# Kernel optimization log

Hardware: AMD Instinct MI355X
Metric: run time of the kernel (lower is better)

Reference implementation:

```python
import jax, jax.numpy as jnp
import numpy as np

F = 256      # n_features
N = 128      # n_nodes
B = 4096     # batch


def setup_inputs() -> dict:
    key = jax.random.key(0)
    ks = jax.random.split(key, 11)
    s = lambda *sh: 1.0 / np.sqrt(sh[-2]) if len(sh) >= 2 else 1.0
    x = jax.random.normal(ks[0], (B, F), dtype=jnp.float32)
    # Block-diagonal weights: [F, in, out] per stage; biases [F, out]
    w1 = jax.random.normal(ks[1], (F, 1, N), dtype=jnp.float32)
    b1 = jax.random.normal(ks[2], (F, N), dtype=jnp.float32) * 0.01
    w2 = jax.random.normal(ks[3], (F, N, N), dtype=jnp.float32) / np.sqrt(N)
    b2 = jax.random.normal(ks[4], (F, N), dtype=jnp.float32) * 0.01
    w3 = jax.random.normal(ks[5], (F, N, N), dtype=jnp.float32) / np.sqrt(N)
    b3 = jax.random.normal(ks[6], (F, N), dtype=jnp.float32) * 0.01
    w4 = jax.random.normal(ks[7], (F, N, 1), dtype=jnp.float32) / np.sqrt(N)
    b4 = jax.random.normal(ks[8], (F, 1), dtype=jnp.float32) * 0.01
    # Final linear: [F, 1] weight, [1] bias
    lr_w = jax.random.normal(ks[9], (F, 1), dtype=jnp.float32) / np.sqrt(F)
    lr_b = jax.random.normal(ks[10], (1,), dtype=jnp.float32) * 0.01
    return {"x": x, "w1": w1, "b1": b1, "w2": w2, "b2": b2,
            "w3": w3, "b3": b3, "w4": w4, "b4": b4,
            "lr_w": lr_w, "lr_b": lr_b}


def reference(x, w1, b1, w2, b2, w3, b3, w4, b4, lr_w, lr_b):
    # Per-feature block-diagonal MLP chain with ReLU between stages.
    # x: [B, F] -> view each feature as a 1-dim input to its own subnet.
    h = x[:, :, None]                                   # [B, F, 1]
    h = jax.nn.relu(jnp.einsum('bfi,fio->bfo', h, w1) + b1)   # [B, F, N]
    h = jax.nn.relu(jnp.einsum('bfi,fio->bfo', h, w2) + b2)   # [B, F, N]
    h = jax.nn.relu(jnp.einsum('bfi,fio->bfo', h, w3) + b3)   # [B, F, N]
    h = jnp.einsum('bfi,fio->bfo', h, w4) + b4                # [B, F, 1]
    x_pre = h[:, :, 0]                                        # [B, F]
    return x_pre @ lr_w + lr_b                                # [B, 1]
```

## Files before the change

kernel.cpp:

```cpp
#include <hip/hip_runtime.h>
#include <hip/hip_bf16.h>

#define F_DIM 256
#define N_DIM 128
#define B_DIM 4096

typedef float f32x4v __attribute__((ext_vector_type(4)));
typedef float f32x16v __attribute__((ext_vector_type(16)));
typedef short s16x8 __attribute__((ext_vector_type(8)));
typedef unsigned int u32x4v __attribute__((ext_vector_type(4)));

#define PIN(x) asm("" : "+v"(x))

__device__ __forceinline__ unsigned short f2bf(float f) {
  union { float f; unsigned u; } v; v.f = f;
  unsigned r = v.u + 0x7fffu + ((v.u >> 16) & 1u);
  return (unsigned short)(r >> 16);
}

__device__ __forceinline__ unsigned pk2(float a, float b) {
  union { __hip_bfloat16 h[2]; unsigned u; } v;
  v.h[0] = __float2bfloat16(a);
  v.h[1] = __float2bfloat16(b);
  return v.u;
}

__device__ __forceinline__ void gload16(const void* g, void* l) {
  __builtin_amdgcn_global_load_lds(
      (const __attribute__((address_space(1))) unsigned int*)g,
      (__attribute__((address_space(3))) unsigned int*)l, 16, 0, 0);
}

__device__ __forceinline__ s16x8 frag1(unsigned d) {
  u32x4v v = {d, 0u, 0u, 0u};
  return __builtin_bit_cast(s16x8, v);
}

struct frag2 { s16x8 lo, hi; };

__device__ __forceinline__ frag2 cvt2(f32x16v a) {
  unsigned P[8];
#pragma unroll
  for (int q = 0; q < 8; ++q)
    P[q] = pk2(fmaxf(a[2 * q], 0.f), fmaxf(a[2 * q + 1], 0.f));
  u32x4v lo = {P[0], P[1], P[2], P[3]};
  u32x4v hh = {P[4], P[5], P[6], P[7]};
  frag2 r;
  r.lo = __builtin_bit_cast(s16x8, lo);
  r.hi = __builtin_bit_cast(s16x8, hh);
  return r;
}

__global__ void prep_w(const float* __restrict__ w2, const float* __restrict__ w3,
                       unsigned int* __restrict__ wTs) {
  __shared__ float tile[128 * 130];
  int m = blockIdx.x;
  const float* src = (m < 256) ? (w2 + (size_t)m * 16384)
                               : (w3 + (size_t)(m - 256) * 16384);
  int t = threadIdx.x;
  for (int k = 0; k < 64; ++k) {
    int idx = k * 256 + t;
    int i = idx >> 7, o = idx & 127;
    tile[o * 130 + i] = src[idx];
  }
  __syncthreads();
  unsigned int* dst = wTs + (size_t)m * 8192;
  for (int k = 0; k < 32; ++k) {
    int idx = k * 256 + t;
    int o = idx >> 6, i2 = idx & 63;
    unsigned pk = (unsigned)f2bf(tile[o * 130 + 2 * i2]) |
                  ((unsigned)f2bf(tile[o * 130 + 2 * i2 + 1]) << 16);
    int w = i2 & 7;
    int i2p = (i2 & ~7) + ((w >> 1) & 1) * 4 + (w & 1) + (((w >> 2) & 1) << 1);
    dst[(o * 64) + (i2p ^ ((o & 15) << 2))] = pk;
  }
}

__global__ void prep_x(const float* __restrict__ x, float* __restrict__ xT) {
  __shared__ float tile[64][65];
  int btile = blockIdx.x & 63;
  int ftile = blockIdx.x >> 6;
  int t = threadIdx.x;
  for (int k = 0; k < 16; ++k) {
    int idx = k * 256 + t;
    int r = idx >> 6, c = idx & 63;
    tile[r][c] = x[(size_t)(btile * 64 + r) * F_DIM + ftile * 64 + c];
  }
  __syncthreads();
  for (int k = 0; k < 16; ++k) {
    int idx = k * 256 + t;
    int fr = idx >> 6, br = idx & 63;
    xT[(size_t)(ftile * 64 + fr) * B_DIM + btile * 64 + br] = tile[br][fr];
  }
}

__global__ __launch_bounds__(256, 2) void mlp_chain(
    const float* __restrict__ xT, const float* __restrict__ w1,
    const float* __restrict__ b1, const float* __restrict__ b2,
    const float* __restrict__ b3, const float* __restrict__ w4,
    const float* __restrict__ b4, const unsigned int* __restrict__ wTs,
    float* __restrict__ xp) {
  __shared__ __align__(16) char Wb[2][128 * 256];
  __shared__ __align__(16) float w4l[N_DIM];

  const int f  = blockIdx.x >> 2;
  const int qt = blockIdx.x & 3;
  const int t  = threadIdx.x;
  const int lane = t & 63, wid = t >> 6;
  const int c32 = lane & 31, hi = lane >> 5;

  {
    const char* s2 = (const char*)(wTs + (size_t)f * 8192);
    const char* s3 = (const char*)(wTs + (size_t)(256 + f) * 8192);
#pragma unroll
    for (int c = 0; c < 8; ++c) {
      int off = (wid * 8 + c) * 1024;
      gload16(s2 + off + lane * 16, &Wb[0][off]);
    }
#pragma unroll
    for (int c = 0; c < 8; ++c) {
      int off = (wid * 8 + c) * 1024;
      gload16(s3 + off + lane * 16, &Wb[1][off]);
    }
    if (t < 32) *(f32x4v*)&w4l[t * 4] = *(const f32x4v*)&w4[f * N_DIM + t * 4];
  }

  unsigned a1d[4], a2d[4], a3d[4];
#pragma unroll
  for (int it = 0; it < 4; ++it) {
    int i = it * 32 + c32;
    float w1v = w1[f * N_DIM + i], b1v = b1[f * N_DIM + i];
    float b2v = b2[f * N_DIM + i], b3v = b3[f * N_DIM + i];
    a1d[it] = hi ? 0u : pk2(w1v, b1v);
    a2d[it] = hi ? 0u : pk2(0.f, b2v);
    a3d[it] = hi ? 0u : pk2(0.f, b3v);
  }
  const float b4f = b4[f];
  const float* xcol = xT + (size_t)f * B_DIM + qt * 1024;
  float* xprow = xp + (size_t)f * B_DIM + qt * 1024;

  const int wbase = c32 * 256 + (((lane & 15) ^ hi) << 4);

  __syncthreads();

  const f32x16v zero = {0.f, 0.f, 0.f, 0.f, 0.f, 0.f, 0.f, 0.f,
                        0.f, 0.f, 0.f, 0.f, 0.f, 0.f, 0.f, 0.f};

  float xvA = xcol[wid * 64 + c32];
  float xvB = xcol[wid * 64 + 32 + c32];
#pragma unroll 1
  for (int itb = 0; itb < 4; ++itb) {
    const int bb = itb * 256 + wid * 64;
    s16x8 BxA = frag1(hi ? 0u : pk2(xvA, 1.0f));
    s16x8 BxB = frag1(hi ? 0u : pk2(xvB, 1.0f));
    float xvA_n = (itb < 3) ? xcol[bb + 256 + c32] : 0.f;
    float xvB_n = (itb < 3) ? xcol[bb + 256 + 32 + c32] : 0.f;

    s16x8 h1A[8], h1B[8];
#pragma unroll
    for (int it = 0; it < 4; ++it) {
      f32x16v hA = __builtin_amdgcn_mfma_f32_32x32x16_bf16(frag1(a1d[it]), BxA,
                                                           zero, 0, 0, 0);
      frag2 rA = cvt2(hA);
      h1A[2 * it] = rA.lo;  h1A[2 * it + 1] = rA.hi;
      PIN(h1A[2 * it]);  PIN(h1A[2 * it + 1]);
      f32x16v hB = __builtin_amdgcn_mfma_f32_32x32x16_bf16(frag1(a1d[it]), BxB,
                                                           zero, 0, 0, 0);
      frag2 rB = cvt2(hB);
      h1B[2 * it] = rB.lo;  h1B[2 * it + 1] = rB.hi;
      PIN(h1B[2 * it]);  PIN(h1B[2 * it + 1]);
    }

    s16x8 h2A[8], h2B[8];
#pragma unroll
    for (int nt = 0; nt < 4; ++nt) {
      f32x16v a2A = __builtin_amdgcn_mfma_f32_32x32x16_bf16(frag1(a2d[nt]), BxA,
                                                            zero, 0, 0, 0);
      f32x16v a2B = __builtin_amdgcn_mfma_f32_32x32x16_bf16(frag1(a2d[nt]), BxB,
                                                            zero, 0, 0, 0);
#pragma unroll
      for (int m = 0; m < 8; ++m) {
        s16x8 af = *(const s16x8*)(&Wb[0][0] + nt * 8192 + (wbase ^ (m << 5)));
        a2A = __builtin_amdgcn_mfma_f32_32x32x16_bf16(af, h1A[m], a2A, 0, 0, 0);
        a2B = __builtin_amdgcn_mfma_f32_32x32x16_bf16(af, h1B[m], a2B, 0, 0, 0);
      }
      frag2 rA = cvt2(a2A);
      h2A[2 * nt] = rA.lo;  h2A[2 * nt + 1] = rA.hi;
      PIN(h2A[2 * nt]);  PIN(h2A[2 * nt + 1]);
      frag2 rB = cvt2(a2B);
      h2B[2 * nt] = rB.lo;  h2B[2 * nt + 1] = rB.hi;
      PIN(h2B[2 * nt]);  PIN(h2B[2 * nt + 1]);
    }

    float pA = 0.f, pB = 0.f;
#pragma unroll
    for (int n3 = 0; n3 < 4; ++n3) {
      f32x16v a3A = __builtin_amdgcn_mfma_f32_32x32x16_bf16(frag1(a3d[n3]), BxA,
                                                            zero, 0, 0, 0);
      f32x16v a3B = __builtin_amdgcn_mfma_f32_32x32x16_bf16(frag1(a3d[n3]), BxB,
                                                            zero, 0, 0, 0);
#pragma unroll
      for (int k = 0; k < 8; ++k) {
        s16x8 af = *(const s16x8*)(&Wb[1][0] + n3 * 8192 + (wbase ^ (k << 5)));
        a3A = __builtin_amdgcn_mfma_f32_32x32x16_bf16(af, h2A[k], a3A, 0, 0, 0);
        a3B = __builtin_amdgcn_mfma_f32_32x32x16_bf16(af, h2B[k], a3B, 0, 0, 0);
      }
#pragma unroll
      for (int q = 0; q < 4; ++q) {
        f32x4v wv = *(const f32x4v*)&w4l[n3 * 32 + q * 8 + hi * 4];
#pragma unroll
        for (int i = 0; i < 4; ++i) {
          pA = fmaf(fmaxf(a3A[4 * q + i], 0.f), wv[i], pA);
          pB = fmaf(fmaxf(a3B[4 * q + i], 0.f), wv[i], pB);
        }
      }
    }
    pA += __shfl_xor(pA, 32, 64);
    pB += __shfl_xor(pB, 32, 64);
    if (hi == 0) {
      xprow[bb + c32]      = pA + b4f;
      xprow[bb + 32 + c32] = pB + b4f;
    }
    xvA = xvA_n;
    xvB = xvB_n;
  }
}

__global__ void final_reduce(const float* __restrict__ xp,
                             const float* __restrict__ lr_w,
                             const float* __restrict__ lr_b,
                             float* __restrict__ out) {
  __shared__ float lw[F_DIM];
  __shared__ float part[4][64];
  int t = threadIdx.x;
  if (t < F_DIM) lw[t] = lr_w[t];
  __syncthreads();
  int q = t >> 6, bl = t & 63;
  int b = blockIdx.x * 64 + bl;
  float acc = 0.f;
#pragma unroll 8
  for (int j = 0; j < 64; ++j) {
    int ff = q * 64 + j;
    acc += xp[(size_t)ff * B_DIM + b] * lw[ff];
  }
  part[q][bl] = acc;
  __syncthreads();
  if (q == 0)
    out[b] = part[0][bl] + part[1][bl] + part[2][bl] + part[3][bl] + lr_b[0];
}

extern "C" void kernel_launch(void* const* d_in, const int* in_sizes, int n_in,
                              void* d_out, int out_size, void* d_ws, size_t ws_size,
                              hipStream_t stream) {
  (void)in_sizes; (void)n_in; (void)out_size; (void)ws_size;
  const float* x    = (const float*)d_in[0];
  const float* w1   = (const float*)d_in[1];
  const float* b1   = (const float*)d_in[2];
  const float* w2   = (const float*)d_in[3];
  const float* b2   = (const float*)d_in[4];
  const float* w3   = (const float*)d_in[5];
  const float* b3   = (const float*)d_in[6];
  const float* w4   = (const float*)d_in[7];
  const float* b4   = (const float*)d_in[8];
  const float* lr_w = (const float*)d_in[9];
  const float* lr_b = (const float*)d_in[10];
  float* out = (float*)d_out;

  char* ws = (char*)d_ws;
  unsigned int* wTs = (unsigned int*)ws;
  float* xT = (float*)(ws + (16u << 20));
  float* xp = (float*)(ws + (16u << 20) + (4u << 20));

  prep_w<<<512, 256, 0, stream>>>(w2, w3, wTs);
  prep_x<<<256, 256, 0, stream>>>(x, xT);
  mlp_chain<<<1024, 256, 0, stream>>>(xT, w1, b1, b2, b3, w4, b4, wTs, xp);
  final_reduce<<<64, 256, 0, stream>>>(xp, lr_w, lr_b, out);
}
```

Baseline: 102.1 us.

## Interleave two output tiles per MFMA chain, raise MFMA priority, pack ReLU

Layers 2 and 3 now process two output column tiles at once, giving four independent MFMA accumulator chains. This hides MFMA dependency latency and shares each h fragment across more MFMAs. s_setprio brackets the MFMA loops so waves issuing matrix work get priority, and the LDS offsets are precomputed and pinned in registers. ReLU is applied after bf16 packing via v_pk_max_i16, which is valid because negative bf16 values compare below zero as signed 16-bit integers. The cost is higher register pressure from the extra live accumulators.

```diff
diff --git a/kernel.cpp b/kernel.cpp
--- a/kernel.cpp
+++ b/kernel.cpp
@@ -41,8 +41,10 @@
 __device__ __forceinline__ frag2 cvt2(f32x16v a) {
   unsigned P[8];
 #pragma unroll
-  for (int q = 0; q < 8; ++q)
-    P[q] = pk2(fmaxf(a[2 * q], 0.f), fmaxf(a[2 * q + 1], 0.f));
+  for (int q = 0; q < 8; ++q) {
+    unsigned pk = pk2(a[2 * q], a[2 * q + 1]);
+    asm("v_pk_max_i16 %0, %1, 0" : "=v"(P[q]) : "v"(pk));
+  }
   u32x4v lo = {P[0], P[1], P[2], P[3]};
   u32x4v hh = {P[4], P[5], P[6], P[7]};
   frag2 r;
@@ -140,6 +142,10 @@
   float* xprow = xp + (size_t)f * B_DIM + qt * 1024;
 
   const int wbase = c32 * 256 + (((lane & 15) ^ hi) << 4);
+  int va[8];
+#pragma unroll
+  for (int m = 0; m < 8; ++m) { va[m] = wbase ^ (m << 5); PIN(va[m]); }
+  const char* wb = &Wb[0][0];
 
   __syncthreads();
 
@@ -173,45 +179,74 @@
 
     s16x8 h2A[8], h2B[8];
 #pragma unroll
-    for (int nt = 0; nt < 4; ++nt) {
-      f32x16v a2A = __builtin_amdgcn_mfma_f32_32x32x16_bf16(frag1(a2d[nt]), BxA,
-                                                            zero, 0, 0, 0);
-      f32x16v a2B = __builtin_amdgcn_mfma_f32_32x32x16_bf16(frag1(a2d[nt]), BxB,
-                                                            zero, 0, 0, 0);
+    for (int ntp = 0; ntp < 2; ++ntp) {
+      const int nt0 = 2 * ntp, nt1 = nt0 + 1;
+      f32x16v u0A = __builtin_amdgcn_mfma_f32_32x32x16_bf16(frag1(a2d[nt0]), BxA,
+                                                            zero, 0, 0, 0);
+      f32x16v u0B = __builtin_amdgcn_mfma_f32_32x32x16_bf16(frag1(a2d[nt0]), BxB,
+                                                            zero, 0, 0, 0);
+      f32x16v u1A = __builtin_amdgcn_mfma_f32_32x32x16_bf16(frag1(a2d[nt1]), BxA,
+                                                            zero, 0, 0, 0);
+      f32x16v u1B = __builtin_amdgcn_mfma_f32_32x32x16_bf16(frag1(a2d[nt1]), BxB,
+                                                            zero, 0, 0, 0);
+      __builtin_amdgcn_s_setprio(1);
 #pragma unroll
       for (int m = 0; m < 8; ++m) {
-        s16x8 af = *(const s16x8*)(&Wb[0][0] + nt * 8192 + (wbase ^ (m << 5)));
-        a2A = __builtin_amdgcn_mfma_f32_32x32x16_bf16(af, h1A[m], a2A, 0, 0, 0);
-        a2B = __builtin_amdgcn_mfma_f32_32x32x16_bf16(af, h1B[m], a2B, 0, 0, 0);
+        s16x8 af0 = *(const s16x8*)(wb + va[m] + nt0 * 8192);
+        s16x8 af1 = *(const s16x8*)(wb + va[m] + nt1 * 8192);
+        u0A = __builtin_amdgcn_mfma_f32_32x32x16_bf16(af0, h1A[m], u0A, 0, 0, 0);
+        u0B = __builtin_amdgcn_mfma_f32_32x32x16_bf16(af0, h1B[m], u0B, 0, 0, 0);
+        u1A = __builtin_amdgcn_mfma_f32_32x32x16_bf16(af1, h1A[m], u1A, 0, 0, 0);
+        u1B = __builtin_amdgcn_mfma_f32_32x32x16_bf16(af1, h1B[m], u1B, 0, 0, 0);
       }
-      frag2 rA = cvt2(a2A);
-      h2A[2 * nt] = rA.lo;  h2A[2 * nt + 1] = rA.hi;
-      PIN(h2A[2 * nt]);  PIN(h2A[2 * nt + 1]);
-      frag2 rB = cvt2(a2B);
-      h2B[2 * nt] = rB.lo;  h2B[2 * nt + 1] = rB.hi;
-      PIN(h2B[2 * nt]);  PIN(h2B[2 * nt + 1]);
+      __builtin_amdgcn_s_setprio(0);
+      frag2 r0A = cvt2(u0A);
+      h2A[2 * nt0] = r0A.lo;  h2A[2 * nt0 + 1] = r0A.hi;
+      PIN(h2A[2 * nt0]);  PIN(h2A[2 * nt0 + 1]);
+      frag2 r0B = cvt2(u0B);
+      h2B[2 * nt0] = r0B.lo;  h2B[2 * nt0 + 1] = r0B.hi;
+      PIN(h2B[2 * nt0]);  PIN(h2B[2 * nt0 + 1]);
+      frag2 r1A = cvt2(u1A);
+      h2A[2 * nt1] = r1A.lo;  h2A[2 * nt1 + 1] = r1A.hi;
+      PIN(h2A[2 * nt1]);  PIN(h2A[2 * nt1 + 1]);
+      frag2 r1B = cvt2(u1B);
+      h2B[2 * nt1] = r1B.lo;  h2B[2 * nt1 + 1] = r1B.hi;
+      PIN(h2B[2 * nt1]);  PIN(h2B[2 * nt1 + 1]);
     }
 
     float pA = 0.f, pB = 0.f;
 #pragma unroll
-    for (int n3 = 0; n3 < 4; ++n3) {
-      f32x16v a3A = __builtin_amdgcn_mfma_f32_32x32x16_bf16(frag1(a3d[n3]), BxA,
-                                                            zero, 0, 0, 0);
-      f32x16v a3B = __builtin_amdgcn_mfma_f32_32x32x16_bf16(frag1(a3d[n3]), BxB,
-                                                            zero, 0, 0, 0);
+    for (int n3p = 0; n3p < 2; ++n3p) {
+      const int n30 = 2 * n3p, n31 = n30 + 1;
+      f32x16v v0A = __builtin_amdgcn_mfma_f32_32x32x16_bf16(frag1(a3d[n30]), BxA,
+                                                            zero, 0, 0, 0);
+      f32x16v v0B = __builtin_amdgcn_mfma_f32_32x32x16_bf16(frag1(a3d[n30]), BxB,
+                                                            zero, 0, 0, 0);
+      f32x16v v1A = __builtin_amdgcn_mfma_f32_32x32x16_bf16(frag1(a3d[n31]), BxA,
+                                                            zero, 0, 0, 0);
+      f32x16v v1B = __builtin_amdgcn_mfma_f32_32x32x16_bf16(frag1(a3d[n31]), BxB,
+                                                            zero, 0, 0, 0);
+      __builtin_amdgcn_s_setprio(1);
 #pragma unroll
       for (int k = 0; k < 8; ++k) {
-        s16x8 af = *(const s16x8*)(&Wb[1][0] + n3 * 8192 + (wbase ^ (k << 5)));
-        a3A = __builtin_amdgcn_mfma_f32_32x32x16_bf16(af, h2A[k], a3A, 0, 0, 0);
-        a3B = __builtin_amdgcn_mfma_f32_32x32x16_bf16(af, h2B[k], a3B, 0, 0, 0);
+        s16x8 af0 = *(const s16x8*)(wb + va[k] + 32768 + n30 * 8192);
+        s16x8 af1 = *(const s16x8*)(wb + va[k] + 32768 + n31 * 8192);
+        v0A = __builtin_amdgcn_mfma_f32_32x32x16_bf16(af0, h2A[k], v0A, 0, 0, 0);
+        v0B = __builtin_amdgcn_mfma_f32_32x32x16_bf16(af0, h2B[k], v0B, 0, 0, 0);
+        v1A = __builtin_amdgcn_mfma_f32_32x32x16_bf16(af1, h2A[k], v1A, 0, 0, 0);
+        v1B = __builtin_amdgcn_mfma_f32_32x32x16_bf16(af1, h2B[k], v1B, 0, 0, 0);
       }
+      __builtin_amdgcn_s_setprio(0);
 #pragma unroll
       for (int q = 0; q < 4; ++q) {
-        f32x4v wv = *(const f32x4v*)&w4l[n3 * 32 + q * 8 + hi * 4];
+        f32x4v wv0 = *(const f32x4v*)&w4l[n30 * 32 + q * 8 + hi * 4];
+        f32x4v wv1 = *(const f32x4v*)&w4l[n31 * 32 + q * 8 + hi * 4];
 #pragma unroll
         for (int i = 0; i < 4; ++i) {
-          pA = fmaf(fmaxf(a3A[4 * q + i], 0.f), wv[i], pA);
-          pB = fmaf(fmaxf(a3B[4 * q + i], 0.f), wv[i], pB);
+          pA = fmaf(fmaxf(v0A[4 * q + i], 0.f), wv0[i], pA);
+          pB = fmaf(fmaxf(v0B[4 * q + i], 0.f), wv0[i], pB);
+          pA = fmaf(fmaxf(v1A[4 * q + i], 0.f), wv1[i], pA);
+          pB = fmaf(fmaxf(v1B[4 * q + i], 0.f), wv1[i], pB);
         }
       }
     }
```

Result: faster. 97.51 us (-4.5%).
